# Kernel tuning notes

Hardware: AMD Instinct MI355X
Metric: run time of the kernel (lower is better)

## Reference

```python
import jax, jax.numpy as jnp
import numpy as np

N_NODES = 100000
N_EDGES = 1600000
NFEAT = 128
NHID = 64
DROPOUT = 0.5


def setup_inputs() -> dict:
    key = jax.random.key(0)
    k1, k2, k3, k4, k5, k6 = jax.random.split(key, 6)
    x = jax.random.normal(k1, (N_NODES, NFEAT), dtype=jnp.float32)
    edge_row = jax.random.randint(k2, (N_EDGES,), 0, N_NODES, dtype=jnp.int32)
    edge_col = jax.random.randint(k3, (N_EDGES,), 0, N_NODES, dtype=jnp.int32)
    edge_val = jax.random.uniform(k4, (N_EDGES,), dtype=jnp.float32)
    # GraphConvolution params (uniform init as in Kipf's reference impl)
    stdv = 1.0 / np.sqrt(NHID)
    W = jax.random.uniform(k5, (NFEAT, NHID), minval=-stdv, maxval=stdv, dtype=jnp.float32)
    b = jax.random.uniform(k6, (NHID,), minval=-stdv, maxval=stdv, dtype=jnp.float32)
    return {"x": x, "edge_row": edge_row, "edge_col": edge_col,
            "edge_val": edge_val, "W": W, "b": b}


def reference(x, edge_row, edge_col, edge_val, W, b):
    # GraphConvolution: support = x @ W ; out = spmm(adj, support) + b
    support = x @ W                                   # [N, nhid]
    msgs = edge_val[:, None] * support[edge_col]       # gather: [E, nhid]
    agg = jax.ops.segment_sum(msgs, edge_row, num_segments=N_NODES)  # scatter-add
    h = jax.nn.relu(agg + b)
    # F.dropout(p=0.5, training=True): inverted dropout with fixed mask
    keep = 1.0 - DROPOUT
    mask = jax.random.bernoulli(jax.random.key(42), keep, h.shape)
    return jnp.where(mask, h / keep, 0.0)
```

## Files before the change

kernel.cpp:

```cpp
#include <hip/hip_runtime.h>

#define N_NODES 100000
#define N_EDGES 1600000
#define NFEAT 128
#define NHID 64

#define BBITS 8
#define NBUCK 391
#define BATCH 4096
#define NBATCH ((N_EDGES + BATCH - 1) / BATCH)
#define CMASK 0x1FFFF

typedef __attribute__((ext_vector_type(8))) short short8;
typedef __attribute__((ext_vector_type(4))) float f32x4;

__device__ __forceinline__ unsigned short f2bf(float f) {
  unsigned u = __float_as_uint(f);
  u += 0x7fffu + ((u >> 16) & 1u);
  return (unsigned short)(u >> 16);
}

__global__ __launch_bounds__(256) void gcn_wt(const float* __restrict__ W,
                                              unsigned short* __restrict__ wt) {
  const int i = blockIdx.x * 256 + threadIdx.x;
  const int n = i >> 7;
  const int k = i & 127;
  wt[i] = f2bf(W[k * NHID + n]);
}

__global__ __launch_bounds__(256) void gcn_gemm(const float* __restrict__ x,
                                                const unsigned short* __restrict__ wt,
                                                unsigned short* __restrict__ support_h) {
  __shared__ float ldsx[64 * NFEAT];
  const int t = threadIdx.x;
  const int node0 = blockIdx.x * 64;
  const float4* __restrict__ gx = (const float4*)(x + (size_t)node0 * NFEAT);
  float4* lx4 = (float4*)ldsx;
  const int limit4 = (N_NODES - node0) * (NFEAT / 4);
#pragma unroll
  for (int i = 0; i < 8; ++i) {
    const int idx = i * 256 + t;
    if (idx < limit4) lx4[idx] = gx[idx];
  }
  __syncthreads();
  const int wv = t >> 6;
  const int lane = t & 63;
  const int quad = lane >> 4;
  const int nl = lane & 15;
  const int mrow = wv * 16 + nl;
  f32x4 acc[4];
#pragma unroll
  for (int nt = 0; nt < 4; ++nt)
#pragma unroll
    for (int r = 0; r < 4; ++r) acc[nt][r] = 0.f;
#pragma unroll
  for (int kc = 0; kc < 4; ++kc) {
    const float* ap = &ldsx[mrow * NFEAT + kc * 32 + quad * 8];
    const float4 a0 = *(const float4*)ap;
    const float4 a1 = *(const float4*)(ap + 4);
    union { short8 v; unsigned short s[8]; } au;
    au.s[0] = f2bf(a0.x); au.s[1] = f2bf(a0.y);
    au.s[2] = f2bf(a0.z); au.s[3] = f2bf(a0.w);
    au.s[4] = f2bf(a1.x); au.s[5] = f2bf(a1.y);
    au.s[6] = f2bf(a1.z); au.s[7] = f2bf(a1.w);
#pragma unroll
    for (int nt = 0; nt < 4; ++nt) {
      const short8 bf = *(const short8*)(wt + (size_t)(nt * 16 + nl) * NFEAT +
                                         kc * 32 + quad * 8);
      acc[nt] = __builtin_amdgcn_mfma_f32_16x16x32_bf16(au.v, bf, acc[nt], 0, 0, 0);
    }
  }
#pragma unroll
  for (int nt = 0; nt < 4; ++nt)
#pragma unroll
    for (int r = 0; r < 4; ++r) {
      const int node = node0 + wv * 16 + quad * 4 + r;
      if (node < N_NODES)
        support_h[(size_t)node * NHID + nt * 16 + nl] = f2bf(acc[nt][r]);
    }
}

__global__ __launch_bounds__(512) void gcn_bucket_hist(const int* __restrict__ erow,
                                                       int* __restrict__ hist_g) {
  __shared__ int h[NBUCK];
  for (int t = threadIdx.x; t < NBUCK; t += 512) h[t] = 0;
  __syncthreads();
  const int base = blockIdx.x * BATCH;
  const int n = min(BATCH, N_EDGES - base);
  for (int j = threadIdx.x; j < n; j += 512)
    atomicAdd(&h[erow[base + j] >> BBITS], 1);
  __syncthreads();
  for (int t = threadIdx.x; t < NBUCK; t += 512)
    hist_g[(size_t)blockIdx.x * NBUCK + t] = h[t];
}

__global__ __launch_bounds__(512) void gcn_colscan(int* __restrict__ hist_g,
                                                   int* __restrict__ tot) {
  __shared__ int sm[512];
  const int k = blockIdx.x;
  const int t = threadIdx.x;
  const int v = (t < NBATCH) ? hist_g[(size_t)t * NBUCK + k] : 0;
  sm[t] = v;
  __syncthreads();
  for (int off = 1; off < 512; off <<= 1) {
    const int xv = (t >= off) ? sm[t - off] : 0;
    __syncthreads();
    sm[t] += xv;
    __syncthreads();
  }
  if (t < NBATCH) hist_g[(size_t)t * NBUCK + k] = sm[t] - v;
  if (t == NBATCH - 1) tot[k] = sm[t];
}

__global__ __launch_bounds__(512) void gcn_bucket_scan(const int* __restrict__ tot,
                                                       int* __restrict__ bstart,
                                                       int* __restrict__ row_start) {
  __shared__ int sm[512];
  const int t = threadIdx.x;
  const int v = (t < NBUCK) ? tot[t] : 0;
  sm[t] = v;
  __syncthreads();
  for (int off = 1; off < 512; off <<= 1) {
    const int xv = (t >= off) ? sm[t - off] : 0;
    __syncthreads();
    sm[t] += xv;
    __syncthreads();
  }
  if (t < NBUCK) bstart[t] = sm[t] - v;
  if (t == NBUCK - 1) bstart[NBUCK] = sm[t];
  if (t == 0) row_start[N_NODES] = N_EDGES;
}

__global__ __launch_bounds__(512) void gcn_bin(const int* __restrict__ erow,
                                               const int* __restrict__ ecol,
                                               const float* __restrict__ eval_,
                                               const int* __restrict__ colofs,
                                               const int* __restrict__ bstart,
                                               int2* __restrict__ eg) {
  __shared__ int h[NBUCK];
  __shared__ int ofs[NBUCK];
  __shared__ int sm[512];
  __shared__ int spx[BATCH];
  __shared__ int sv[BATCH];
  __shared__ short sb[BATCH];
  const int t = threadIdx.x;
  for (int i = t; i < NBUCK; i += 512) h[i] = 0;
  __syncthreads();
  const int base = blockIdx.x * BATCH;
  const int n = min(BATCH, N_EDGES - base);
  int mypx[8], myv[8], myrank[8], myb[8];
#pragma unroll
  for (int u = 0; u < 8; ++u) {
    const int j = t + u * 512;
    if (j < n) {
      const int r = erow[base + j];
      mypx[u] = ((r & 255) << 17) | ecol[base + j];
      myv[u] = __float_as_int(eval_[base + j]);
      myb[u] = r >> BBITS;
      myrank[u] = atomicAdd(&h[myb[u]], 1);
    }
  }
  __syncthreads();
  const int hv = (t < NBUCK) ? h[t] : 0;
  sm[t] = hv;
  __syncthreads();
  for (int off = 1; off < 512; off <<= 1) {
    const int xv = (t >= off) ? sm[t - off] : 0;
    __syncthreads();
    sm[t] += xv;
    __syncthreads();
  }
  if (t < NBUCK) ofs[t] = sm[t] - hv;
  __syncthreads();
#pragma unroll
  for (int u = 0; u < 8; ++u) {
    const int j = t + u * 512;
    if (j < n) {
      const int pos = ofs[myb[u]] + myrank[u];
      spx[pos] = mypx[u];
      sv[pos] = myv[u];
      sb[pos] = (short)myb[u];
    }
  }
  if (t < NBUCK) h[t] = bstart[t] + colofs[(size_t)blockIdx.x * NBUCK + t] - ofs[t];
  __syncthreads();
  for (int j = t; j < n; j += 512) {
    const int d = h[sb[j]] + j;
    eg[d] = make_int2(spx[j], sv[j]);
  }
}

__global__ __launch_bounds__(512) void gcn_rowsort(const int* __restrict__ bstart,
                                                   int2* __restrict__ eg,
                                                   int* __restrict__ row_start) {
  __shared__ int cnt[256];
  __shared__ int sm[256];
  __shared__ int rofs[256];
  const int t = threadIdx.x;
  const int k = blockIdx.x;
  if (t < 256) cnt[t] = 0;
  __syncthreads();
  const int s = bstart[k];
  const int n = bstart[k + 1] - s;
  int px[9], pv[9], rk[9];
#pragma unroll
  for (int u = 0; u < 9; ++u) {
    const int j = t + u * 512;
    if (j < n) {
      const int2 p = eg[s + j];
      px[u] = p.x;
      pv[u] = p.y;
      rk[u] = atomicAdd(&cnt[p.x >> 17], 1);
    }
  }
  __syncthreads();
  const int myc = (t < 256) ? cnt[t] : 0;
  if (t < 256) sm[t] = myc;
  __syncthreads();
  for (int off = 1; off < 256; off <<= 1) {
    int xv = 0;
    if (t >= off && t < 256) xv = sm[t - off];
    __syncthreads();
    if (t < 256) sm[t] += xv;
    __syncthreads();
  }
  if (t < 256) {
    rofs[t] = sm[t] - myc;
    const int node = (k << BBITS) + t;
    if (node < N_NODES) row_start[node] = s + sm[t] - myc;
  }
  __syncthreads();
#pragma unroll
  for (int u = 0; u < 9; ++u) {
    const int j = t + u * 512;
    if (j < n) {
      const int d = s + rofs[px[u] >> 17] + rk[u];
      eg[d] = make_int2(px[u] & CMASK, pv[u]);
    }
  }
}

__device__ __forceinline__ unsigned rotl32(unsigned v, int r) {
  return (v << r) | (v >> (32 - r));
}

__device__ __forceinline__ unsigned threefry_draw(unsigned i) {
  const unsigned ks0 = 0u;
  const unsigned ks1 = 42u;
  const unsigned ks2 = 0x1BD11BDAu ^ 42u;
  unsigned x0 = 0u + ks0;
  unsigned x1 = i + ks1;
#define TF_ROUND(r) { x0 += x1; x1 = rotl32(x1, (r)); x1 ^= x0; }
  TF_ROUND(13) TF_ROUND(15) TF_ROUND(26) TF_ROUND(6)
  x0 += ks1; x1 += ks2 + 1u;
  TF_ROUND(17) TF_ROUND(29) TF_ROUND(16) TF_ROUND(24)
  x0 += ks2; x1 += ks0 + 2u;
  TF_ROUND(13) TF_ROUND(15) TF_ROUND(26) TF_ROUND(6)
  x0 += ks0; x1 += ks1 + 3u;
  TF_ROUND(17) TF_ROUND(29) TF_ROUND(16) TF_ROUND(24)
  x0 += ks1; x1 += ks2 + 4u;
  TF_ROUND(13) TF_ROUND(15) TF_ROUND(26) TF_ROUND(6)
  x0 += ks2; x1 += ks0 + 5u;
#undef TF_ROUND
  return x0 ^ x1;
}

__global__ __launch_bounds__(256) void gcn_aggregate(const int* __restrict__ row_start,
                                                     const int2* __restrict__ eg,
                                                     const unsigned short* __restrict__ support_h,
                                                     const float* __restrict__ b,
                                                     float* __restrict__ out) {
  const int node = (int)((blockIdx.x * 256u + threadIdx.x) >> 6);
  const int lane = threadIdx.x & 63;
  const int grp = lane >> 3;
  const int sub = lane & 7;
  const int s = row_start[node];
  const int e = row_start[node + 1];
  float acc[8];
#pragma unroll
  for (int j = 0; j < 8; ++j) acc[j] = 0.f;
  for (int i = s; i < e; i += 8) {
    const int idx = i + grp;
    const int2 p = (idx < e) ? eg[idx] : make_int2(0, 0);
    const uint4 q = ((const uint4*)support_h)[(size_t)p.x * 8 + sub];
    const float v = __int_as_float(p.y);
    acc[0] = __builtin_fmaf(v, __uint_as_float(q.x << 16), acc[0]);
    acc[1] = __builtin_fmaf(v, __uint_as_float(q.x & 0xffff0000u), acc[1]);
    acc[2] = __builtin_fmaf(v, __uint_as_float(q.y << 16), acc[2]);
    acc[3] = __builtin_fmaf(v, __uint_as_float(q.y & 0xffff0000u), acc[3]);
    acc[4] = __builtin_fmaf(v, __uint_as_float(q.z << 16), acc[4]);
    acc[5] = __builtin_fmaf(v, __uint_as_float(q.z & 0xffff0000u), acc[5]);
    acc[6] = __builtin_fmaf(v, __uint_as_float(q.w << 16), acc[6]);
    acc[7] = __builtin_fmaf(v, __uint_as_float(q.w & 0xffff0000u), acc[7]);
  }
  const int g0 = grp & 1, g1 = (grp >> 1) & 1, g2 = grp >> 2;
  float v4[4];
#pragma unroll
  for (int i = 0; i < 4; ++i) {
    const float keep = g0 ? acc[2 * i + 1] : acc[2 * i];
    const float give = g0 ? acc[2 * i] : acc[2 * i + 1];
    v4[i] = keep + __shfl_xor(give, 8);
  }
  float v2[2];
#pragma unroll
  for (int i = 0; i < 2; ++i) {
    const float keep = g1 ? v4[2 * i + 1] : v4[2 * i];
    const float give = g1 ? v4[2 * i] : v4[2 * i + 1];
    v2[i] = keep + __shfl_xor(give, 16);
  }
  const float keep = g2 ? v2[1] : v2[0];
  const float give = g2 ? v2[0] : v2[1];
  const float aval = keep + __shfl_xor(give, 32);
  const int feat = (sub << 3) | grp;
  const float h = fmaxf(aval + b[feat], 0.f);
  const unsigned idxg = (unsigned)node * 64u + (unsigned)feat;
  const bool keepm = (threefry_draw(idxg) >> 31) == 0u;
  out[idxg] = keepm ? h * 2.0f : 0.0f;
}

extern "C" void kernel_launch(void* const* d_in, const int* in_sizes, int n_in,
                              void* d_out, int out_size, void* d_ws, size_t ws_size,
                              hipStream_t stream) {
  const float* x     = (const float*)d_in[0];
  const int*   erow  = (const int*)d_in[1];
  const int*   ecol  = (const int*)d_in[2];
  const float* eval_ = (const float*)d_in[3];
  const float* W     = (const float*)d_in[4];
  const float* b     = (const float*)d_in[5];
  float* out = (float*)d_out;

  char* ws = (char*)d_ws;
  unsigned short* support_h = (unsigned short*)(ws);
  unsigned short* wt        = (unsigned short*)(ws + 12800000);
  int2*  eg       = (int2*)(ws + 25600000);
  int*   hist_g   = (int*)(ws + 38400000);
  int*   tot      = (int*)(ws + 39011536);
  int*   bstart   = (int*)(ws + 39013104);
  int*   row_start= (int*)(ws + 39014672);

  hipLaunchKernelGGL(gcn_wt, dim3(32), dim3(256), 0, stream, W, wt);
  hipLaunchKernelGGL(gcn_gemm, dim3((N_NODES + 63) / 64), dim3(256), 0, stream,
                     x, wt, support_h);
  hipLaunchKernelGGL(gcn_bucket_hist, dim3(NBATCH), dim3(512), 0, stream, erow, hist_g);
  hipLaunchKernelGGL(gcn_colscan, dim3(NBUCK), dim3(512), 0, stream, hist_g, tot);
  hipLaunchKernelGGL(gcn_bucket_scan, dim3(1), dim3(512), 0, stream, tot, bstart, row_start);
  hipLaunchKernelGGL(gcn_bin, dim3(NBATCH), dim3(512), 0, stream,
                     erow, ecol, eval_, hist_g, bstart, eg);
  hipLaunchKernelGGL(gcn_rowsort, dim3(NBUCK), dim3(512), 0, stream,
                     bstart, eg, row_start);
  hipLaunchKernelGGL(gcn_aggregate, dim3(N_NODES / 4), dim3(256), 0, stream,
                     row_start, eg, support_h, b, out);
}
```

Before: 211.6 us.

## Replace histogram-scan bucketing with fixed-stride buckets and atomic cursors

Drops the three kernels that built the bucket histogram and its column and bucket prefix sums. Each bucket now gets a fixed-capacity slot region (STRIDE) and a padded global cursor. Each bin block reserves its space with one atomicAdd per bucket. The bucket width shrinks to 128 rows, the batch size drops to 2048, and rowsort now writes to a separate output array using LDS atomic cursors. This removes a pass over edge_row and several launches. In exchange it assumes no bucket exceeds 2432 edges, which holds for uniformly random rows but would corrupt memory on skewed graphs. It also makes the within-row edge order, and so the float summation order, nondeterministic.

```diff
diff --git a/kernel.cpp b/kernel.cpp
--- a/kernel.cpp
+++ b/kernel.cpp
@@ -5,10 +5,11 @@
 #define NFEAT 128
 #define NHID 64
 
-#define BBITS 8
-#define NBUCK 391
-#define BATCH 4096
+#define BBITS 7
+#define NBUCK 782
+#define BATCH 2048
 #define NBATCH ((N_EDGES + BATCH - 1) / BATCH)
+#define STRIDE 2432
 #define CMASK 0x1FFFF
 
 typedef __attribute__((ext_vector_type(8))) short short8;
@@ -21,11 +22,15 @@
 }
 
 __global__ __launch_bounds__(256) void gcn_wt(const float* __restrict__ W,
-                                              unsigned short* __restrict__ wt) {
+                                              unsigned short* __restrict__ wt,
+                                              int* __restrict__ cursor) {
   const int i = blockIdx.x * 256 + threadIdx.x;
   const int n = i >> 7;
   const int k = i & 127;
   wt[i] = f2bf(W[k * NHID + n]);
+  if (blockIdx.x == 0)
+    for (int b = threadIdx.x; b < NBUCK; b += 256)
+      cursor[b * 16] = b * STRIDE;
 }
 
 __global__ __launch_bounds__(256) void gcn_gemm(const float* __restrict__ x,
@@ -80,62 +85,10 @@
     }
 }
 
-__global__ __launch_bounds__(512) void gcn_bucket_hist(const int* __restrict__ erow,
-                                                       int* __restrict__ hist_g) {
-  __shared__ int h[NBUCK];
-  for (int t = threadIdx.x; t < NBUCK; t += 512) h[t] = 0;
-  __syncthreads();
-  const int base = blockIdx.x * BATCH;
-  const int n = min(BATCH, N_EDGES - base);
-  for (int j = threadIdx.x; j < n; j += 512)
-    atomicAdd(&h[erow[base + j] >> BBITS], 1);
-  __syncthreads();
-  for (int t = threadIdx.x; t < NBUCK; t += 512)
-    hist_g[(size_t)blockIdx.x * NBUCK + t] = h[t];
-}
-
-__global__ __launch_bounds__(512) void gcn_colscan(int* __restrict__ hist_g,
-                                                   int* __restrict__ tot) {
-  __shared__ int sm[512];
-  const int k = blockIdx.x;
-  const int t = threadIdx.x;
-  const int v = (t < NBATCH) ? hist_g[(size_t)t * NBUCK + k] : 0;
-  sm[t] = v;
-  __syncthreads();
-  for (int off = 1; off < 512; off <<= 1) {
-    const int xv = (t >= off) ? sm[t - off] : 0;
-    __syncthreads();
-    sm[t] += xv;
-    __syncthreads();
-  }
-  if (t < NBATCH) hist_g[(size_t)t * NBUCK + k] = sm[t] - v;
-  if (t == NBATCH - 1) tot[k] = sm[t];
-}
-
-__global__ __launch_bounds__(512) void gcn_bucket_scan(const int* __restrict__ tot,
-                                                       int* __restrict__ bstart,
-                                                       int* __restrict__ row_start) {
-  __shared__ int sm[512];
-  const int t = threadIdx.x;
-  const int v = (t < NBUCK) ? tot[t] : 0;
-  sm[t] = v;
-  __syncthreads();
-  for (int off = 1; off < 512; off <<= 1) {
-    const int xv = (t >= off) ? sm[t - off] : 0;
-    __syncthreads();
-    sm[t] += xv;
-    __syncthreads();
-  }
-  if (t < NBUCK) bstart[t] = sm[t] - v;
-  if (t == NBUCK - 1) bstart[NBUCK] = sm[t];
-  if (t == 0) row_start[N_NODES] = N_EDGES;
-}
-
 __global__ __launch_bounds__(512) void gcn_bin(const int* __restrict__ erow,
                                                const int* __restrict__ ecol,
                                                const float* __restrict__ eval_,
-                                               const int* __restrict__ colofs,
-                                               const int* __restrict__ bstart,
+                                               int* __restrict__ cursor,
                                                int2* __restrict__ eg) {
   __shared__ int h[NBUCK];
   __shared__ int ofs[NBUCK];
@@ -148,21 +101,24 @@
   __syncthreads();
   const int base = blockIdx.x * BATCH;
   const int n = min(BATCH, N_EDGES - base);
-  int mypx[8], myv[8], myrank[8], myb[8];
-#pragma unroll
-  for (int u = 0; u < 8; ++u) {
+  int mypx[4], myv[4], myrank[4], myb[4];
+#pragma unroll
+  for (int u = 0; u < 4; ++u) {
     const int j = t + u * 512;
     if (j < n) {
       const int r = erow[base + j];
-      mypx[u] = ((r & 255) << 17) | ecol[base + j];
+      mypx[u] = ((r & 127) << 17) | ecol[base + j];
       myv[u] = __float_as_int(eval_[base + j]);
       myb[u] = r >> BBITS;
       myrank[u] = atomicAdd(&h[myb[u]], 1);
     }
   }
   __syncthreads();
-  const int hv = (t < NBUCK) ? h[t] : 0;
-  sm[t] = hv;
+  const int k0 = 2 * t, k1 = 2 * t + 1;
+  const int a0 = (k0 < NBUCK) ? h[k0] : 0;
+  const int a1 = (k1 < NBUCK) ? h[k1] : 0;
+  const int lsum = a0 + a1;
+  sm[t] = lsum;
   __syncthreads();
   for (int off = 1; off < 512; off <<= 1) {
     const int xv = (t >= off) ? sm[t - off] : 0;
@@ -170,10 +126,12 @@
     sm[t] += xv;
     __syncthreads();
   }
-  if (t < NBUCK) ofs[t] = sm[t] - hv;
-  __syncthreads();
-#pragma unroll
-  for (int u = 0; u < 8; ++u) {
+  const int excl = sm[t] - lsum;
+  if (k0 < NBUCK) ofs[k0] = excl;
+  if (k1 < NBUCK) ofs[k1] = excl + a0;
+  __syncthreads();
+#pragma unroll
+  for (int u = 0; u < 4; ++u) {
     const int j = t + u * 512;
     if (j < n) {
       const int pos = ofs[myb[u]] + myrank[u];
@@ -182,7 +140,13 @@
       sb[pos] = (short)myb[u];
     }
   }
-  if (t < NBUCK) h[t] = bstart[t] + colofs[(size_t)blockIdx.x * NBUCK + t] - ofs[t];
+  for (int i = t; i < NBUCK; i += 512) {
+    const int c = h[i];
+    if (c > 0) {
+      const int gb = atomicAdd(&cursor[i * 16], c);
+      h[i] = gb - ofs[i];
+    }
+  }
   __syncthreads();
   for (int j = t; j < n; j += 512) {
     const int d = h[sb[j]] + j;
@@ -190,53 +154,45 @@
   }
 }
 
-__global__ __launch_bounds__(512) void gcn_rowsort(const int* __restrict__ bstart,
-                                                   int2* __restrict__ eg,
-                                                   int* __restrict__ row_start) {
-  __shared__ int cnt[256];
-  __shared__ int sm[256];
-  __shared__ int rofs[256];
+__global__ __launch_bounds__(512) void gcn_rowsort(const int* __restrict__ cursor,
+                                                   const int2* __restrict__ eg,
+                                                   int2* __restrict__ eg2,
+                                                   int2* __restrict__ rs_re) {
+  __shared__ int cnt[128];
+  __shared__ int sm[128];
+  __shared__ int cur[128];
   const int t = threadIdx.x;
   const int k = blockIdx.x;
-  if (t < 256) cnt[t] = 0;
-  __syncthreads();
-  const int s = bstart[k];
-  const int n = bstart[k + 1] - s;
-  int px[9], pv[9], rk[9];
-#pragma unroll
-  for (int u = 0; u < 9; ++u) {
-    const int j = t + u * 512;
-    if (j < n) {
-      const int2 p = eg[s + j];
-      px[u] = p.x;
-      pv[u] = p.y;
-      rk[u] = atomicAdd(&cnt[p.x >> 17], 1);
-    }
-  }
-  __syncthreads();
-  const int myc = (t < 256) ? cnt[t] : 0;
-  if (t < 256) sm[t] = myc;
-  __syncthreads();
-  for (int off = 1; off < 256; off <<= 1) {
+  const int bbase = k * STRIDE;
+  const int n = cursor[k * 16] - bbase;
+  if (t < 128) cnt[t] = 0;
+  __syncthreads();
+  const int* egx = (const int*)eg;
+  for (int j = t; j < n; j += 512)
+    atomicAdd(&cnt[((unsigned)egx[(size_t)(bbase + j) * 2]) >> 17], 1);
+  __syncthreads();
+  const int myc = (t < 128) ? cnt[t] : 0;
+  if (t < 128) sm[t] = myc;
+  __syncthreads();
+  for (int off = 1; off < 128; off <<= 1) {
     int xv = 0;
-    if (t >= off && t < 256) xv = sm[t - off];
+    if (t >= off && t < 128) xv = sm[t - off];
     __syncthreads();
-    if (t < 256) sm[t] += xv;
+    if (t < 128) sm[t] += xv;
     __syncthreads();
   }
-  if (t < 256) {
-    rofs[t] = sm[t] - myc;
+  if (t < 128) {
+    const int start = bbase + sm[t] - myc;
+    cur[t] = start;
     const int node = (k << BBITS) + t;
-    if (node < N_NODES) row_start[node] = s + sm[t] - myc;
-  }
-  __syncthreads();
-#pragma unroll
-  for (int u = 0; u < 9; ++u) {
-    const int j = t + u * 512;
-    if (j < n) {
-      const int d = s + rofs[px[u] >> 17] + rk[u];
-      eg[d] = make_int2(px[u] & CMASK, pv[u]);
-    }
+    if (node < N_NODES) rs_re[node] = make_int2(start, start + myc);
+  }
+  __syncthreads();
+  for (int j = t; j < n; j += 512) {
+    const int2 p = eg[bbase + j];
+    const int row = ((unsigned)p.x) >> 17;
+    const int d = atomicAdd(&cur[row], 1);
+    eg2[d] = make_int2(p.x & CMASK, p.y);
   }
 }
 
@@ -265,8 +221,8 @@
   return x0 ^ x1;
 }
 
-__global__ __launch_bounds__(256) void gcn_aggregate(const int* __restrict__ row_start,
-                                                     const int2* __restrict__ eg,
+__global__ __launch_bounds__(256) void gcn_aggregate(const int2* __restrict__ rs_re,
+                                                     const int2* __restrict__ eg2,
                                                      const unsigned short* __restrict__ support_h,
                                                      const float* __restrict__ b,
                                                      float* __restrict__ out) {
@@ -274,14 +230,15 @@
   const int lane = threadIdx.x & 63;
   const int grp = lane >> 3;
   const int sub = lane & 7;
-  const int s = row_start[node];
-  const int e = row_start[node + 1];
+  const int2 se = rs_re[node];
+  const int s = se.x;
+  const int e = se.y;
   float acc[8];
 #pragma unroll
   for (int j = 0; j < 8; ++j) acc[j] = 0.f;
   for (int i = s; i < e; i += 8) {
     const int idx = i + grp;
-    const int2 p = (idx < e) ? eg[idx] : make_int2(0, 0);
+    const int2 p = (idx < e) ? eg2[idx] : make_int2(0, 0);
     const uint4 q = ((const uint4*)support_h)[(size_t)p.x * 8 + sub];
     const float v = __int_as_float(p.y);
     acc[0] = __builtin_fmaf(v, __uint_as_float(q.x << 16), acc[0]);
@@ -332,22 +289,18 @@
   char* ws = (char*)d_ws;
   unsigned short* support_h = (unsigned short*)(ws);
   unsigned short* wt        = (unsigned short*)(ws + 12800000);
-  int2*  eg       = (int2*)(ws + 25600000);
-  int*   hist_g   = (int*)(ws + 38400000);
-  int*   tot      = (int*)(ws + 39011536);
-  int*   bstart   = (int*)(ws + 39013104);
-  int*   row_start= (int*)(ws + 39014672);
-
-  hipLaunchKernelGGL(gcn_wt, dim3(32), dim3(256), 0, stream, W, wt);
+  int2* rs_re   = (int2*)(ws + 12816384);
+  int*  cursor  = (int*)(ws + 13616384);
+  int2* eg      = (int2*)(ws + 13666432);
+  int2* eg2     = (int2*)(ws + 28881024);
+
+  hipLaunchKernelGGL(gcn_wt, dim3(32), dim3(256), 0, stream, W, wt, cursor);
   hipLaunchKernelGGL(gcn_gemm, dim3((N_NODES + 63) / 64), dim3(256), 0, stream,
                      x, wt, support_h);
-  hipLaunchKernelGGL(gcn_bucket_hist, dim3(NBATCH), dim3(512), 0, stream, erow, hist_g);
-  hipLaunchKernelGGL(gcn_colscan, dim3(NBUCK), dim3(512), 0, stream, hist_g, tot);
-  hipLaunchKernelGGL(gcn_bucket_scan, dim3(1), dim3(512), 0, stream, tot, bstart, row_start);
   hipLaunchKernelGGL(gcn_bin, dim3(NBATCH), dim3(512), 0, stream,
-                     erow, ecol, eval_, hist_g, bstart, eg);
+                     erow, ecol, eval_, cursor, eg);
   hipLaunchKernelGGL(gcn_rowsort, dim3(NBUCK), dim3(512), 0, stream,
-                     bstart, eg, row_start);
+                     cursor, eg, eg2, rs_re);
   hipLaunchKernelGGL(gcn_aggregate, dim3(N_NODES / 4), dim3(256), 0, stream,
-                     row_start, eg, support_h, b, out);
-}
+                     rs_re, eg2, support_h, b, out);
+}
```

Measured after the change: 235.3 us. +11.2%, slower.
